# Optimization experiments

Hardware: AMD Instinct MI355X
Metric: run time of the kernel (lower is better)

The kernel has to match this reference:

```python
import jax, jax.numpy as jnp
import numpy as np

B, S, D, H = 2, 2048, 768, 12
DH = D // H  # head dim = 64


def setup_inputs() -> dict:
    key = jax.random.key(0)
    ks = jax.random.split(key, 4)
    query = jax.random.normal(ks[0], (B, S, D), dtype=jnp.float32)
    # right-padding: positions >= length are padded (True = masked)
    lengths = jax.random.randint(ks[1], (B,), S // 2, S + 1)
    padding_mask = jnp.arange(S)[None, :] >= lengths[:, None]
    w_qkv = jax.random.normal(ks[2], (3 * D, D), dtype=jnp.float32) * 0.02
    b_qkv = jnp.zeros((3 * D,), dtype=jnp.float32)
    w_out = jax.random.normal(ks[3], (D, D), dtype=jnp.float32) * 0.02
    b_out = jnp.zeros((D,), dtype=jnp.float32)
    return {"query": query, "padding_mask": padding_mask, "w_qkv": w_qkv,
            "b_qkv": b_qkv, "w_out": w_out, "b_out": b_out}


def reference(query, padding_mask, w_qkv, b_qkv, w_out, b_out):
    # qkv_same self-attention path, future_mask=True, dropout in eval mode.
    qkv = query @ w_qkv.T + b_qkv                       # [B,S,3D]
    q, k, v = jnp.split(qkv, 3, axis=-1)
    split = lambda x: x.reshape(B, S, H, DH).transpose(0, 2, 1, 3)  # [B,H,S,dh]
    q, k, v = split(q), split(k), split(v)
    scale = jnp.float32(1.0 / np.sqrt(DH))
    w = jnp.einsum('bhqd,bhkd->bhqk', q, k) * scale     # [B,H,S,S]
    neg_inf = jnp.float32(-jnp.inf)
    causal = jnp.triu(jnp.ones((S, S), dtype=bool), 1)  # strict upper = future
    w = jnp.where(causal[None, None], neg_inf, w)
    w = jnp.where(padding_mask[:, None, None, :], neg_inf, w)
    # rows where every key is masked -> output zeros (matches torch cleanup)
    all_masked = jnp.all(jnp.isneginf(w), axis=-1)      # [B,H,S]
    w = jnp.where(all_masked[..., None], 0.0, w)        # avoid NaN in softmax
    p = jax.nn.softmax(w, axis=-1)
    p = jnp.where(all_masked[..., None], 0.0, p)
    out = jnp.einsum('bhqk,bhkd->bhqd', p, v)           # [B,H,S,dh]
    out = out.transpose(0, 2, 1, 3).reshape(B, S, D)
    return out @ w_out.T + b_out
```

## Files before the change

kernel.cpp:

```cpp
#include <hip/hip_runtime.h>

#define BATCH 2
#define SEQ 2048
#define DMODEL 768
#define NH 12
#define DHEAD 64
#define D3 (3 * DMODEL)

typedef float f32x4 __attribute__((ext_vector_type(4)));
typedef __bf16 bf16x8 __attribute__((ext_vector_type(8)));
typedef __bf16 bf16x4 __attribute__((ext_vector_type(4)));

#define NEG_INF (-__builtin_inff())
#define SCL 0.18033688011112042f

__device__ __forceinline__ void g2l16(const void* g, void* l) {
    __builtin_amdgcn_global_load_lds(
        (const __attribute__((address_space(1))) void*)g,
        (__attribute__((address_space(3))) void*)l,
        16, 0, 0);
}

__device__ __forceinline__ unsigned pack_bf16(float lo, float hi) {
    unsigned a = __builtin_bit_cast(unsigned short, (__bf16)lo);
    unsigned b = __builtin_bit_cast(unsigned short, (__bf16)hi);
    return a | (b << 16);
}

#define XQ 786432
#define WQQ 442368
#define WOQ 147456
#define WQROWS 147456
__global__ __launch_bounds__(256) void cvt3_kernel(const float* __restrict__ X,
                                                   const float* __restrict__ Wq,
                                                   const float* __restrict__ Wo,
                                                   __bf16* __restrict__ Xb,
                                                   __bf16* __restrict__ Wqb,
                                                   __bf16* __restrict__ Wob) {
    int i = blockIdx.x * 256 + threadIdx.x;
    const float* s; __bf16* d; int k;
    float scl = 1.0f;
    if (i < XQ)            { s = X;  d = Xb;  k = i; }
    else if (i < XQ + WQQ) { s = Wq; d = Wqb; k = i - XQ; if (k < WQROWS) scl = SCL; }
    else                   { s = Wo; d = Wob; k = i - XQ - WQQ; }
    float4 v = ((const float4*)s)[k];
    bf16x4 o;
    o[0] = (__bf16)(v.x * scl); o[1] = (__bf16)(v.y * scl);
    o[2] = (__bf16)(v.z * scl); o[3] = (__bf16)(v.w * scl);
    ((bf16x4*)d)[k] = o;
}

__global__ __launch_bounds__(256) void lens_kernel(const unsigned char* __restrict__ mask,
                                                   const float* __restrict__ bq,
                                                   float* __restrict__ bqs,
                                                   int* __restrict__ lens) {
    __shared__ int nz_s;
    __shared__ int cnt[2];
    if (threadIdx.x == 0) { nz_s = 0; cnt[0] = 0; cnt[1] = 0; }
    __syncthreads();
    for (int i = threadIdx.x; i < D3; i += 256)
        bqs[i] = bq[i] * (i < DMODEL ? SCL : 1.0f);
    uint4 mv = ((const uint4*)mask)[threadIdx.x];
    if (mv.x | mv.y | mv.z | mv.w) nz_s = 1;
    __syncthreads();
    int c0 = 0, c1 = 0;
    if (nz_s) {
        for (int s = threadIdx.x; s < SEQ; s += 256) {
            c0 += (mask[s] != 0);
            c1 += (mask[SEQ + s] != 0);
        }
    } else {
        const int* mi = (const int*)mask;
        for (int s = threadIdx.x; s < SEQ; s += 256) {
            c0 += (mi[s] != 0);
            c1 += (mi[SEQ + s] != 0);
        }
    }
    atomicAdd(&cnt[0], c0);
    atomicAdd(&cnt[1], c1);
    __syncthreads();
    if (threadIdx.x == 0) {
        lens[0] = SEQ - cnt[0];
        lens[1] = SEQ - cnt[1];
    }
}

__global__ __launch_bounds__(256) void gemm_qkv(const __bf16* __restrict__ A,
                                                const __bf16* __restrict__ Bw,
                                                const float* __restrict__ bias,
                                                __bf16* __restrict__ Qd,
                                                __bf16* __restrict__ Kd,
                                                __bf16* __restrict__ Vd) {
    const int K = 768, N = 2304;
    __shared__ __align__(16) __bf16 As[128][64];
    __shared__ __align__(16) __bf16 Bs[128][64];
    const int tid = threadIdx.x;
    const int wave = tid >> 6, lane = tid & 63;
    const int bm = blockIdx.x * 128, bn = blockIdx.y * 128;
    const int wr = (wave >> 1) * 64, wc = (wave & 1) * 64;
    const int l15 = lane & 15, lg = lane >> 4;
    const int rsub = lane >> 3;
    const int csub = (((lane & 7) ^ rsub) * 8);
    const int rswz = (l15 & 7) * 8;

    f32x4 acc[4][4] = {};

    for (int kt = 0; kt < K; kt += 64) {
#pragma unroll
        for (int it = 0; it < 4; ++it) {
            int c = it * 4 + wave;
            int row = c * 8 + rsub;
            g2l16(A + (size_t)(bm + row) * K + kt + csub, &As[0][0] + c * 512);
            g2l16(Bw + (size_t)(bn + row) * K + kt + csub, &Bs[0][0] + c * 512);
        }
        __syncthreads();
#pragma unroll
        for (int kk = 0; kk < 2; ++kk) {
            bf16x8 af[4], bfr[4];
            const int col = (kk * 32 + lg * 8) ^ rswz;
#pragma unroll
            for (int m = 0; m < 4; ++m)
                af[m] = *(const bf16x8*)(&As[0][0] + (wr + m * 16 + l15) * 64 + col);
#pragma unroll
            for (int n = 0; n < 4; ++n)
                bfr[n] = *(const bf16x8*)(&Bs[0][0] + (wc + n * 16 + l15) * 64 + col);
#pragma unroll
            for (int m = 0; m < 4; ++m)
#pragma unroll
                for (int n = 0; n < 4; ++n)
                    acc[m][n] = __builtin_amdgcn_mfma_f32_16x16x32_bf16(af[m], bfr[n], acc[m][n], 0, 0, 0);
        }
        __syncthreads();
    }

#pragma unroll
    for (int n = 0; n < 4; ++n) {
        int col = bn + wc + n * 16 + l15;
        float bv = bias[col];
#pragma unroll
        for (int m = 0; m < 4; ++m) {
#pragma unroll
            for (int j = 0; j < 4; ++j) {
                int row = bm + wr + m * 16 + lg * 4 + j;
                __bf16 v = (__bf16)(acc[m][n][j] + bv);
                if (bn < 768) {
                    Qd[(size_t)row * 768 + col] = v;
                } else if (bn < 1536) {
                    int kc = col - 768;
                    int hh = kc >> 6, dh = kc & 63;
                    int bb = row >> 11, key = row & 2047;
                    Kd[(size_t)(bb * NH + hh) * 131072 + key * 64 + dh] = v;
                } else {
                    Vd[(size_t)row * 768 + (col - 1536)] = v;
                }
            }
        }
    }
    (void)N;
}

__global__ __launch_bounds__(256) void gemm_out(const __bf16* __restrict__ A,
                                                const __bf16* __restrict__ Bw,
                                                const float* __restrict__ bias,
                                                float* __restrict__ Cout,
                                                int M, int N, int K) {
    __shared__ __align__(16) __bf16 As[128][64];
    __shared__ __align__(16) __bf16 Bs[128][64];
    const int tid = threadIdx.x;
    const int wave = tid >> 6, lane = tid & 63;
    const int bm = blockIdx.x * 128, bn = blockIdx.y * 128;
    const int wr = (wave >> 1) * 64, wc = (wave & 1) * 64;
    const int l15 = lane & 15, lg = lane >> 4;
    const int rsub = lane >> 3;
    const int csub = (((lane & 7) ^ rsub) * 8);
    const int rswz = (l15 & 7) * 8;

    f32x4 acc[4][4] = {};

    for (int kt = 0; kt < K; kt += 64) {
#pragma unroll
        for (int it = 0; it < 4; ++it) {
            int c = it * 4 + wave;
            int row = c * 8 + rsub;
            g2l16(A + (size_t)(bm + row) * K + kt + csub, &As[0][0] + c * 512);
            g2l16(Bw + (size_t)(bn + row) * K + kt + csub, &Bs[0][0] + c * 512);
        }
        __syncthreads();
#pragma unroll
        for (int kk = 0; kk < 2; ++kk) {
            bf16x8 af[4], bfr[4];
            const int col = (kk * 32 + lg * 8) ^ rswz;
#pragma unroll
            for (int m = 0; m < 4; ++m)
                af[m] = *(const bf16x8*)(&As[0][0] + (wr + m * 16 + l15) * 64 + col);
#pragma unroll
            for (int n = 0; n < 4; ++n)
                bfr[n] = *(const bf16x8*)(&Bs[0][0] + (wc + n * 16 + l15) * 64 + col);
#pragma unroll
            for (int m = 0; m < 4; ++m)
#pragma unroll
                for (int n = 0; n < 4; ++n)
                    acc[m][n] = __builtin_amdgcn_mfma_f32_16x16x32_bf16(af[m], bfr[n], acc[m][n], 0, 0, 0);
        }
        __syncthreads();
    }

#pragma unroll
    for (int n = 0; n < 4; ++n) {
        int col = bn + wc + n * 16 + l15;
        float bv = bias[col];
#pragma unroll
        for (int m = 0; m < 4; ++m) {
#pragma unroll
            for (int j = 0; j < 4; ++j) {
                int row = bm + wr + m * 16 + lg * 4 + j;
                Cout[(size_t)row * N + col] = acc[m][n][j] + bv;
            }
        }
    }
}

__global__ __launch_bounds__(256) void vtr_kernel(const __bf16* __restrict__ Vd,
                                                  __bf16* __restrict__ Vp) {
    __shared__ __align__(16) __bf16 T[64][72];
    const int bh = blockIdx.x, st = blockIdx.y;
    const int b = bh / NH, h = bh % NH;
    const int s0 = st * 64;
    const __bf16* src = Vd + (size_t)(b * SEQ + s0) * DMODEL + h * DHEAD;
    const int t = threadIdx.x;
    {
        int s = t >> 2, c0 = (t & 3) * 16;
        const __bf16* p = src + (size_t)s * DMODEL + c0;
        *(bf16x8*)&T[s][c0] = *(const bf16x8*)p;
        *(bf16x8*)&T[s][c0 + 8] = *(const bf16x8*)(p + 8);
    }
    __syncthreads();
    {
        int dh = t >> 2, sc4 = (t & 3) * 16;
        bf16x8 o0, o1;
#pragma unroll
        for (int i = 0; i < 8; ++i) o0[i] = T[sc4 + i][dh];
#pragma unroll
        for (int i = 0; i < 8; ++i) o1[i] = T[sc4 + 8 + i][dh];
        __bf16* q = Vp + (size_t)bh * 131072 + st * 4096 + dh * 64 + sc4;
        *(bf16x8*)q = o0;
        *(bf16x8*)(q + 8) = o1;
    }
}

__global__ __launch_bounds__(64) void attn_kernel(const __bf16* __restrict__ Qd,
                                                  const __bf16* __restrict__ Kd,
                                                  const int* __restrict__ lens,
                                                  const __bf16* __restrict__ Vp,
                                                  __bf16* __restrict__ Out) {
    const int lane = threadIdx.x;
    const int l15 = lane & 15, lg = lane >> 4;
    const int blk = blockIdx.x;
    const int xcd = blk & 7, idx = blk >> 3;
    const int hl = idx % 3, pd = idx / 3;
    const int p = 63 - pd;
    const int bh = xcd * 3 + hl;
    const int b = bh / NH, h = bh % NH;
    const int len = lens[b];
    const int q0 = p * 32;

    const int prow = ((l15 >> 2) << 3) + (l15 & 3);
    const __bf16* kbase = Kd + (size_t)bh * 131072 + prow * 64 + lg * 8;
    const __bf16* vbase = Vp + (size_t)bh * 131072 + l15 * 64 + lg * 8;

    bf16x8 qf[2][2];
    int qcap[2];
#pragma unroll
    for (int m = 0; m < 2; ++m) {
        const __bf16* qp_ = Qd + (size_t)(b * SEQ + q0 + m * 16 + l15) * DMODEL + h * DHEAD + lg * 8;
        qf[m][0] = *(const bf16x8*)qp_;
        qf[m][1] = *(const bf16x8*)(qp_ + 32);
        int myq = q0 + m * 16 + l15;
        qcap[m] = (len - 1 < myq) ? (len - 1) : myq;
    }

    int kmax = q0 + 32;
    if (len < kmax) kmax = len;
    const int nt = (kmax + 63) >> 6;

    f32x4 accO[2][4] = {};
    float l_part[2] = {0.f, 0.f};

    bf16x8 kA[2][4], kB[2][4];

    auto kload = [&](bf16x8(&kf)[2][4], int kt) {
        const int k0 = kt * 64;
#pragma unroll
        for (int n = 0; n < 4; ++n) {
            const int roff = (k0 + ((n >> 1) << 5) + ((n & 1) << 2)) * 64;
#pragma unroll
            for (int kkd = 0; kkd < 2; ++kkd)
                kf[kkd][n] = *(const bf16x8*)(kbase + roff + kkd * 32);
        }
    };

    auto compute = [&](bf16x8(&kf)[2][4], int kt) {
        const int k0 = kt * 64;
        const __bf16* vt = vbase + kt * 4096;
        bf16x8 vf[2][4];
#pragma unroll
        for (int kk = 0; kk < 2; ++kk)
#pragma unroll
            for (int n = 0; n < 4; ++n)
                vf[kk][n] = *(const bf16x8*)(vt + n * 1024 + kk * 32);

        bf16x8 pa[2][2];
#pragma unroll
        for (int m = 0; m < 2; ++m) {
            f32x4 sc[4] = {};
            __builtin_amdgcn_s_setprio(1);
#pragma unroll
            for (int n = 0; n < 4; ++n) {
                sc[n] = __builtin_amdgcn_mfma_f32_16x16x32_bf16(kf[0][n], qf[m][0], sc[n], 0, 0, 0);
                sc[n] = __builtin_amdgcn_mfma_f32_16x16x32_bf16(kf[1][n], qf[m][1], sc[n], 0, 0, 0);
            }
            __builtin_amdgcn_s_setprio(0);

            const bool full = (k0 + 63 <= q0 + m * 16) && (k0 + 63 < len);
            float psum = 0.f;
            unsigned pk[4][2];
#pragma unroll
            for (int n = 0; n < 4; ++n) {
                const int keyb = k0 + ((n >> 1) << 5) + lg * 8 + ((n & 1) << 2);
                float pv[4];
#pragma unroll
                for (int j = 0; j < 4; ++j) {
                    float e = exp2f(sc[n][j]);
                    if (!full) e = (keyb + j <= qcap[m]) ? e : 0.f;
                    pv[j] = e;
                }
                psum += (pv[0] + pv[1]) + (pv[2] + pv[3]);
                pk[n][0] = pack_bf16(pv[0], pv[1]);
                pk[n][1] = pack_bf16(pv[2], pv[3]);
            }
            l_part[m] += psum;

            uint4 u0 = {pk[0][0], pk[0][1], pk[1][0], pk[1][1]};
            uint4 u1 = {pk[2][0], pk[2][1], pk[3][0], pk[3][1]};
            pa[m][0] = __builtin_bit_cast(bf16x8, u0);
            pa[m][1] = __builtin_bit_cast(bf16x8, u1);
        }

        __builtin_amdgcn_s_setprio(1);
#pragma unroll
        for (int m = 0; m < 2; ++m)
#pragma unroll
            for (int kk = 0; kk < 2; ++kk)
#pragma unroll
                for (int n = 0; n < 4; ++n)
                    accO[m][n] = __builtin_amdgcn_mfma_f32_16x16x32_bf16(pa[m][kk], vf[kk][n], accO[m][n], 0, 0, 0);
        __builtin_amdgcn_s_setprio(0);
    };

    kload(kA, 0);
    int kt = 0;
    for (;;) {
        if (kt + 1 < nt) kload(kB, kt + 1);
        compute(kA, kt);
        ++kt; if (kt == nt) break;
        if (kt + 1 < nt) kload(kA, kt + 1);
        compute(kB, kt);
        ++kt; if (kt == nt) break;
    }

#pragma unroll
    for (int m = 0; m < 2; ++m) {
        float lp = l_part[m];
        lp += __shfl_xor(lp, 16);
        lp += __shfl_xor(lp, 32);
        float inv = 1.0f / lp;
        float inv_j[4];
#pragma unroll
        for (int j = 0; j < 4; ++j) inv_j[j] = __shfl(inv, lg * 4 + j);
#pragma unroll
        for (int n = 0; n < 4; ++n)
#pragma unroll
            for (int j = 0; j < 4; ++j) {
                int q = q0 + m * 16 + lg * 4 + j;
                Out[(size_t)(b * SEQ + q) * DMODEL + h * DHEAD + n * 16 + l15] =
                    (__bf16)(accO[m][n][j] * inv_j[j]);
            }
    }
}

extern "C" void kernel_launch(void* const* d_in, const int* in_sizes, int n_in,
                              void* d_out, int out_size, void* d_ws, size_t ws_size,
                              hipStream_t stream) {
    const float* query = (const float*)d_in[0];
    const unsigned char* mask = (const unsigned char*)d_in[1];
    const float* w_qkv = (const float*)d_in[2];
    const float* b_qkv = (const float*)d_in[3];
    const float* w_out = (const float*)d_in[4];
    const float* b_out = (const float*)d_in[5];
    float* out = (float*)d_out;

    if (ws_size < 36200448ull) return;
    char* p = (char*)d_ws;
    int* lens = (int*)p;        p += 256;
    float* bqs = (float*)p;     p += 2304 * 4 + 256;
    __bf16* Xb = (__bf16*)p;    p += (size_t)4096 * 768 * 2;
    __bf16* Wqb = (__bf16*)p;   p += (size_t)2304 * 768 * 2;
    __bf16* Wob = (__bf16*)p;   p += (size_t)768 * 768 * 2;
    __bf16* Qd = (__bf16*)p;    p += (size_t)4096 * 768 * 2;
    __bf16* Kd = (__bf16*)p;    p += (size_t)4096 * 768 * 2;
    __bf16* Vd = (__bf16*)p;    p += (size_t)4096 * 768 * 2;
    __bf16* AOb = (__bf16*)p;   p += (size_t)4096 * 768 * 2;
    __bf16* Vpb = Xb;

    lens_kernel<<<1, 256, 0, stream>>>(mask, b_qkv, bqs, lens);
    cvt3_kernel<<<(XQ + WQQ + WOQ) / 256, 256, 0, stream>>>(query, w_qkv, w_out, Xb, Wqb, Wob);

    gemm_qkv<<<dim3(32, 18), 256, 0, stream>>>(Xb, Wqb, bqs, Qd, Kd, Vd);
    vtr_kernel<<<dim3(24, 32), 256, 0, stream>>>(Vd, Vpb);
    attn_kernel<<<1536, 64, 0, stream>>>(Qd, Kd, lens, Vpb, AOb);
    gemm_out<<<dim3(32, 6), 256, 0, stream>>>(AOb, Wob, b_out, out, 4096, 768, 768);
}
```

Baseline: 138.0 us.

## Split long causal query tiles across key ranges and write V pre-transposed

Query tiles in the second half of the sequence are split into 2 or 4 key-range chunks, so each attention block does more even work, and the grid doubles. Partial outputs and row sums for split tiles go to fp32 buffers via atomic adds, and a new normalization kernel then writes bf16. The QKV GEMM now writes V directly into the transposed per-head layout, which removes the separate transpose kernel. The cost is memsets, atomic traffic and strided V stores. It relies on the softmax having no running-max rescaling, so partial sums can simply be added.

```diff
diff --git a/kernel.cpp b/kernel.cpp
--- a/kernel.cpp
+++ b/kernel.cpp
@@ -90,8 +90,8 @@
                                                 const float* __restrict__ bias,
                                                 __bf16* __restrict__ Qd,
                                                 __bf16* __restrict__ Kd,
-                                                __bf16* __restrict__ Vd) {
-    const int K = 768, N = 2304;
+                                                __bf16* __restrict__ Vp) {
+    const int K = 768;
     __shared__ __align__(16) __bf16 As[128][64];
     __shared__ __align__(16) __bf16 Bs[128][64];
     const int tid = threadIdx.x;
@@ -151,12 +151,14 @@
                     int bb = row >> 11, key = row & 2047;
                     Kd[(size_t)(bb * NH + hh) * 131072 + key * 64 + dh] = v;
                 } else {
-                    Vd[(size_t)row * 768 + (col - 1536)] = v;
+                    int vc = col - 1536;
+                    int hh = vc >> 6, dh = vc & 63;
+                    int bb = row >> 11, key = row & 2047;
+                    Vp[(size_t)(bb * NH + hh) * 131072 + (key >> 6) * 4096 + dh * 64 + (key & 63)] = v;
                 }
             }
         }
     }
-    (void)N;
 }
 
 __global__ __launch_bounds__(256) void gemm_out(const __bf16* __restrict__ A,
@@ -220,45 +222,37 @@
     }
 }
 
-__global__ __launch_bounds__(256) void vtr_kernel(const __bf16* __restrict__ Vd,
-                                                  __bf16* __restrict__ Vp) {
-    __shared__ __align__(16) __bf16 T[64][72];
-    const int bh = blockIdx.x, st = blockIdx.y;
-    const int b = bh / NH, h = bh % NH;
-    const int s0 = st * 64;
-    const __bf16* src = Vd + (size_t)(b * SEQ + s0) * DMODEL + h * DHEAD;
-    const int t = threadIdx.x;
-    {
-        int s = t >> 2, c0 = (t & 3) * 16;
-        const __bf16* p = src + (size_t)s * DMODEL + c0;
-        *(bf16x8*)&T[s][c0] = *(const bf16x8*)p;
-        *(bf16x8*)&T[s][c0 + 8] = *(const bf16x8*)(p + 8);
-    }
-    __syncthreads();
-    {
-        int dh = t >> 2, sc4 = (t & 3) * 16;
-        bf16x8 o0, o1;
-#pragma unroll
-        for (int i = 0; i < 8; ++i) o0[i] = T[sc4 + i][dh];
-#pragma unroll
-        for (int i = 0; i < 8; ++i) o1[i] = T[sc4 + 8 + i][dh];
-        __bf16* q = Vp + (size_t)bh * 131072 + st * 4096 + dh * 64 + sc4;
-        *(bf16x8*)q = o0;
-        *(bf16x8*)(q + 8) = o1;
-    }
+__global__ __launch_bounds__(256) void norml_kernel(const float* __restrict__ Oacc,
+                                                    const float* __restrict__ Lacc,
+                                                    __bf16* __restrict__ AOb) {
+    int i = blockIdx.x * 256 + threadIdx.x;
+    int cq = i % 192, row = i / 192;
+    int col = cq * 4;
+    float linv = 1.0f / Lacc[row * NH + (col >> 6)];
+    f32x4 v = ((const f32x4*)Oacc)[i];
+    int b = row >> 10, qr = row & 1023;
+    bf16x4 o;
+    o[0] = (__bf16)(v[0] * linv); o[1] = (__bf16)(v[1] * linv);
+    o[2] = (__bf16)(v[2] * linv); o[3] = (__bf16)(v[3] * linv);
+    *(bf16x4*)(AOb + ((size_t)(b * SEQ + 1024 + qr)) * DMODEL + col) = o;
 }
 
 __global__ __launch_bounds__(64) void attn_kernel(const __bf16* __restrict__ Qd,
                                                   const __bf16* __restrict__ Kd,
                                                   const int* __restrict__ lens,
                                                   const __bf16* __restrict__ Vp,
-                                                  __bf16* __restrict__ Out) {
+                                                  __bf16* __restrict__ Out,
+                                                  float* __restrict__ Oacc,
+                                                  float* __restrict__ Lacc) {
     const int lane = threadIdx.x;
     const int l15 = lane & 15, lg = lane >> 4;
     const int blk = blockIdx.x;
     const int xcd = blk & 7, idx = blk >> 3;
-    const int hl = idx % 3, pd = idx / 3;
-    const int p = 63 - pd;
+    const int hl = idx % 3, item = idx / 3;
+    int p, s, ns;
+    if (item < 32)      { p = 31 - item;            s = 0;            ns = 1; }
+    else if (item < 64) { int t = item - 32; p = 32 + (t >> 1); s = t & 1; ns = 2; }
+    else                { int t = item - 64; p = 48 + (t >> 2); s = t & 3; ns = 4; }
     const int bh = xcd * 3 + hl;
     const int b = bh / NH, h = bh % NH;
     const int len = lens[b];
@@ -282,6 +276,7 @@
     int kmax = q0 + 32;
     if (len < kmax) kmax = len;
     const int nt = (kmax + 63) >> 6;
+    const int ts = (nt * s) / ns, te = (nt * (s + 1)) / ns;
 
     f32x4 accO[2][4] = {};
     float l_part[2] = {0.f, 0.f};
@@ -357,34 +352,56 @@
         __builtin_amdgcn_s_setprio(0);
     };
 
-    kload(kA, 0);
-    int kt = 0;
+    kload(kA, ts);
+    int kt = ts;
     for (;;) {
-        if (kt + 1 < nt) kload(kB, kt + 1);
+        if (kt + 1 < te) kload(kB, kt + 1);
         compute(kA, kt);
-        ++kt; if (kt == nt) break;
-        if (kt + 1 < nt) kload(kA, kt + 1);
+        ++kt; if (kt == te) break;
+        if (kt + 1 < te) kload(kA, kt + 1);
         compute(kB, kt);
-        ++kt; if (kt == nt) break;
-    }
-
-#pragma unroll
-    for (int m = 0; m < 2; ++m) {
-        float lp = l_part[m];
-        lp += __shfl_xor(lp, 16);
-        lp += __shfl_xor(lp, 32);
-        float inv = 1.0f / lp;
-        float inv_j[4];
-#pragma unroll
-        for (int j = 0; j < 4; ++j) inv_j[j] = __shfl(inv, lg * 4 + j);
-#pragma unroll
-        for (int n = 0; n < 4; ++n)
-#pragma unroll
-            for (int j = 0; j < 4; ++j) {
-                int q = q0 + m * 16 + lg * 4 + j;
-                Out[(size_t)(b * SEQ + q) * DMODEL + h * DHEAD + n * 16 + l15] =
-                    (__bf16)(accO[m][n][j] * inv_j[j]);
+        ++kt; if (kt == te) break;
+    }
+
+    if (ns == 1) {
+#pragma unroll
+        for (int m = 0; m < 2; ++m) {
+            float lp = l_part[m];
+            lp += __shfl_xor(lp, 16);
+            lp += __shfl_xor(lp, 32);
+            float inv = 1.0f / lp;
+            float inv_j[4];
+#pragma unroll
+            for (int j = 0; j < 4; ++j) inv_j[j] = __shfl(inv, lg * 4 + j);
+#pragma unroll
+            for (int n = 0; n < 4; ++n)
+#pragma unroll
+                for (int j = 0; j < 4; ++j) {
+                    int q = q0 + m * 16 + lg * 4 + j;
+                    Out[(size_t)(b * SEQ + q) * DMODEL + h * DHEAD + n * 16 + l15] =
+                        (__bf16)(accO[m][n][j] * inv_j[j]);
+                }
+        }
+    } else {
+#pragma unroll
+        for (int m = 0; m < 2; ++m) {
+            float lp = l_part[m];
+            lp += __shfl_xor(lp, 16);
+            lp += __shfl_xor(lp, 32);
+            if (lg == 0) {
+                int q = q0 + m * 16 + l15;
+                unsafeAtomicAdd(&Lacc[(size_t)((b << 10) + (q - 1024)) * NH + h], lp);
             }
+#pragma unroll
+            for (int n = 0; n < 4; ++n)
+#pragma unroll
+                for (int j = 0; j < 4; ++j) {
+                    int q = q0 + m * 16 + lg * 4 + j;
+                    unsafeAtomicAdd(&Oacc[(size_t)((b << 10) + (q - 1024)) * DMODEL +
+                                          h * DHEAD + n * 16 + l15],
+                                    accO[m][n][j]);
+                }
+        }
     }
 }
 
@@ -408,15 +425,20 @@
     __bf16* Wob = (__bf16*)p;   p += (size_t)768 * 768 * 2;
     __bf16* Qd = (__bf16*)p;    p += (size_t)4096 * 768 * 2;
     __bf16* Kd = (__bf16*)p;    p += (size_t)4096 * 768 * 2;
-    __bf16* Vd = (__bf16*)p;    p += (size_t)4096 * 768 * 2;
+    __bf16* Vp = (__bf16*)p;    p += (size_t)4096 * 768 * 2;
     __bf16* AOb = (__bf16*)p;   p += (size_t)4096 * 768 * 2;
-    __bf16* Vpb = Xb;
+    float* Oacc = (float*)Xb;
+    float* Lacc = (float*)Wqb;
 
     lens_kernel<<<1, 256, 0, stream>>>(mask, b_qkv, bqs, lens);
     cvt3_kernel<<<(XQ + WQQ + WOQ) / 256, 256, 0, stream>>>(query, w_qkv, w_out, Xb, Wqb, Wob);
 
-    gemm_qkv<<<dim3(32, 18), 256, 0, stream>>>(Xb, Wqb, bqs, Qd, Kd, Vd);
-    vtr_kernel<<<dim3(24, 32), 256, 0, stream>>>(Vd, Vpb);
-    attn_kernel<<<1536, 64, 0, stream>>>(Qd, Kd, lens, Vpb, AOb);
+    gemm_qkv<<<dim3(32, 18), 256, 0, stream>>>(Xb, Wqb, bqs, Qd, Kd, Vp);
+
+    hipMemsetAsync(Oacc, 0, (size_t)2048 * 768 * 4, stream);
+    hipMemsetAsync(Lacc, 0, (size_t)2048 * NH * 4, stream);
+
+    attn_kernel<<<3072, 64, 0, stream>>>(Qd, Kd, lens, Vp, AOb, Oacc, Lacc);
+    norml_kernel<<<1536, 256, 0, stream>>>(Oacc, Lacc, AOb);
     gemm_out<<<dim3(32, 6), 256, 0, stream>>>(AOb, Wob, b_out, out, 4096, 768, 768);
 }
```

Result: slower. 144.9 us (+5.0%).

## Fuse V transpose into QKV GEMM epilogue and software-pipeline QK MFMA

Applied to the files above, without the earlier changes.

The QKV GEMM epilogue now writes V directly in the tiled, transposed per-head layout that attention consumes, so the separate vtr_kernel launch and its extra global round trip go away. The attention kernel runs two waves per 128-thread block, each handling a different query tile. It also computes the QK^T scores for the next key tile before the softmax/PV step of the current one, to overlap MFMA work with exp and packing. The costs are more scattered stores in the GEMM epilogue and extra registers for the double-buffered score tiles.

```diff
diff --git a/kernel.cpp b/kernel.cpp
--- a/kernel.cpp
+++ b/kernel.cpp
@@ -90,8 +90,8 @@
                                                 const float* __restrict__ bias,
                                                 __bf16* __restrict__ Qd,
                                                 __bf16* __restrict__ Kd,
-                                                __bf16* __restrict__ Vd) {
-    const int K = 768, N = 2304;
+                                                __bf16* __restrict__ Vp) {
+    const int K = 768;
     __shared__ __align__(16) __bf16 As[128][64];
     __shared__ __align__(16) __bf16 Bs[128][64];
     const int tid = threadIdx.x;
@@ -151,12 +151,14 @@
                     int bb = row >> 11, key = row & 2047;
                     Kd[(size_t)(bb * NH + hh) * 131072 + key * 64 + dh] = v;
                 } else {
-                    Vd[(size_t)row * 768 + (col - 1536)] = v;
+                    int vc = col - 1536;
+                    int hh = vc >> 6, dh = vc & 63;
+                    int bb = row >> 11, key = row & 2047;
+                    Vp[(size_t)(bb * NH + hh) * 131072 + (key >> 6) * 4096 + dh * 64 + (key & 63)] = v;
                 }
             }
         }
     }
-    (void)N;
 }
 
 __global__ __launch_bounds__(256) void gemm_out(const __bf16* __restrict__ A,
@@ -220,45 +222,17 @@
     }
 }
 
-__global__ __launch_bounds__(256) void vtr_kernel(const __bf16* __restrict__ Vd,
-                                                  __bf16* __restrict__ Vp) {
-    __shared__ __align__(16) __bf16 T[64][72];
-    const int bh = blockIdx.x, st = blockIdx.y;
-    const int b = bh / NH, h = bh % NH;
-    const int s0 = st * 64;
-    const __bf16* src = Vd + (size_t)(b * SEQ + s0) * DMODEL + h * DHEAD;
-    const int t = threadIdx.x;
-    {
-        int s = t >> 2, c0 = (t & 3) * 16;
-        const __bf16* p = src + (size_t)s * DMODEL + c0;
-        *(bf16x8*)&T[s][c0] = *(const bf16x8*)p;
-        *(bf16x8*)&T[s][c0 + 8] = *(const bf16x8*)(p + 8);
-    }
-    __syncthreads();
-    {
-        int dh = t >> 2, sc4 = (t & 3) * 16;
-        bf16x8 o0, o1;
-#pragma unroll
-        for (int i = 0; i < 8; ++i) o0[i] = T[sc4 + i][dh];
-#pragma unroll
-        for (int i = 0; i < 8; ++i) o1[i] = T[sc4 + 8 + i][dh];
-        __bf16* q = Vp + (size_t)bh * 131072 + st * 4096 + dh * 64 + sc4;
-        *(bf16x8*)q = o0;
-        *(bf16x8*)(q + 8) = o1;
-    }
-}
-
-__global__ __launch_bounds__(64) void attn_kernel(const __bf16* __restrict__ Qd,
-                                                  const __bf16* __restrict__ Kd,
-                                                  const int* __restrict__ lens,
-                                                  const __bf16* __restrict__ Vp,
-                                                  __bf16* __restrict__ Out) {
-    const int lane = threadIdx.x;
+__global__ __launch_bounds__(128) void attn_kernel(const __bf16* __restrict__ Qd,
+                                                   const __bf16* __restrict__ Kd,
+                                                   const int* __restrict__ lens,
+                                                   const __bf16* __restrict__ Vp,
+                                                   __bf16* __restrict__ Out) {
+    const int lane = threadIdx.x & 63, wave = threadIdx.x >> 6;
     const int l15 = lane & 15, lg = lane >> 4;
     const int blk = blockIdx.x;
     const int xcd = blk & 7, idx = blk >> 3;
-    const int hl = idx % 3, pd = idx / 3;
-    const int p = 63 - pd;
+    const int hl = idx % 3, pd2 = idx / 3;
+    const int p = 63 - (pd2 * 2 + wave);
     const int bh = xcd * 3 + hl;
     const int b = bh / NH, h = bh % NH;
     const int len = lens[b];
@@ -287,6 +261,7 @@
     float l_part[2] = {0.f, 0.f};
 
     bf16x8 kA[2][4], kB[2][4];
+    f32x4 scA[2][4], scB[2][4];
 
     auto kload = [&](bf16x8(&kf)[2][4], int kt) {
         const int k0 = kt * 64;
@@ -299,7 +274,20 @@
         }
     };
 
-    auto compute = [&](bf16x8(&kf)[2][4], int kt) {
+    auto qk = [&](f32x4(&sc)[2][4], bf16x8(&kf)[2][4]) {
+        __builtin_amdgcn_s_setprio(1);
+#pragma unroll
+        for (int m = 0; m < 2; ++m)
+#pragma unroll
+            for (int n = 0; n < 4; ++n) {
+                sc[m][n] = __builtin_amdgcn_mfma_f32_16x16x32_bf16(kf[0][n], qf[m][0],
+                                                                   f32x4{0.f, 0.f, 0.f, 0.f}, 0, 0, 0);
+                sc[m][n] = __builtin_amdgcn_mfma_f32_16x16x32_bf16(kf[1][n], qf[m][1], sc[m][n], 0, 0, 0);
+            }
+        __builtin_amdgcn_s_setprio(0);
+    };
+
+    auto step = [&](f32x4(&sc)[2][4], int kt) {
         const int k0 = kt * 64;
         const __bf16* vt = vbase + kt * 4096;
         bf16x8 vf[2][4];
@@ -312,15 +300,6 @@
         bf16x8 pa[2][2];
 #pragma unroll
         for (int m = 0; m < 2; ++m) {
-            f32x4 sc[4] = {};
-            __builtin_amdgcn_s_setprio(1);
-#pragma unroll
-            for (int n = 0; n < 4; ++n) {
-                sc[n] = __builtin_amdgcn_mfma_f32_16x16x32_bf16(kf[0][n], qf[m][0], sc[n], 0, 0, 0);
-                sc[n] = __builtin_amdgcn_mfma_f32_16x16x32_bf16(kf[1][n], qf[m][1], sc[n], 0, 0, 0);
-            }
-            __builtin_amdgcn_s_setprio(0);
-
             const bool full = (k0 + 63 <= q0 + m * 16) && (k0 + 63 < len);
             float psum = 0.f;
             unsigned pk[4][2];
@@ -330,7 +309,7 @@
                 float pv[4];
 #pragma unroll
                 for (int j = 0; j < 4; ++j) {
-                    float e = exp2f(sc[n][j]);
+                    float e = exp2f(sc[m][n][j]);
                     if (!full) e = (keyb + j <= qcap[m]) ? e : 0.f;
                     pv[j] = e;
                 }
@@ -358,14 +337,27 @@
     };
 
     kload(kA, 0);
-    int kt = 0;
+    qk(scA, kA);
+    if (nt > 1) kload(kB, 1);
+
+    int t = 0;
     for (;;) {
-        if (kt + 1 < nt) kload(kB, kt + 1);
-        compute(kA, kt);
-        ++kt; if (kt == nt) break;
-        if (kt + 1 < nt) kload(kA, kt + 1);
-        compute(kB, kt);
-        ++kt; if (kt == nt) break;
+        {
+            const bool hasN = (t + 1 < nt);
+            if (hasN) qk(scB, kB);
+            if (t + 2 < nt) kload(kA, t + 2);
+            step(scA, t);
+            ++t;
+            if (!hasN) break;
+        }
+        {
+            const bool hasN = (t + 1 < nt);
+            if (hasN) qk(scA, kA);
+            if (t + 2 < nt) kload(kB, t + 2);
+            step(scB, t);
+            ++t;
+            if (!hasN) break;
+        }
     }
 
 #pragma unroll
@@ -408,15 +400,13 @@
     __bf16* Wob = (__bf16*)p;   p += (size_t)768 * 768 * 2;
     __bf16* Qd = (__bf16*)p;    p += (size_t)4096 * 768 * 2;
     __bf16* Kd = (__bf16*)p;    p += (size_t)4096 * 768 * 2;
-    __bf16* Vd = (__bf16*)p;    p += (size_t)4096 * 768 * 2;
+    __bf16* Vp = (__bf16*)p;    p += (size_t)4096 * 768 * 2;
     __bf16* AOb = (__bf16*)p;   p += (size_t)4096 * 768 * 2;
-    __bf16* Vpb = Xb;
 
     lens_kernel<<<1, 256, 0, stream>>>(mask, b_qkv, bqs, lens);
     cvt3_kernel<<<(XQ + WQQ + WOQ) / 256, 256, 0, stream>>>(query, w_qkv, w_out, Xb, Wqb, Wob);
 
-    gemm_qkv<<<dim3(32, 18), 256, 0, stream>>>(Xb, Wqb, bqs, Qd, Kd, Vd);
-    vtr_kernel<<<dim3(24, 32), 256, 0, stream>>>(Vd, Vpb);
-    attn_kernel<<<1536, 64, 0, stream>>>(Qd, Kd, lens, Vpb, AOb);
+    gemm_qkv<<<dim3(32, 18), 256, 0, stream>>>(Xb, Wqb, bqs, Qd, Kd, Vp);
+    attn_kernel<<<768, 128, 0, stream>>>(Qd, Kd, lens, Vp, AOb);
     gemm_out<<<dim3(32, 6), 256, 0, stream>>>(AOb, Wob, b_out, out, 4096, 768, 768);
 }
```

Measured after the change: 135.0 us. 2.2% less time.
